# Performance work log

Hardware: AMD Instinct MI355X
Metric: run time of the kernel (lower is better)

Reference implementation:

```python
import jax, jax.numpy as jnp
import numpy as np

B, S, D, H, DQ, DK = 2, 2048, 1024, 16, 64, 64


def setup_inputs() -> dict:
    key = jax.random.key(0)
    ks = jax.random.split(key, 11)
    s = 0.02
    return {
        "query": jax.random.normal(ks[0], (B, S, D), jnp.float32),
        "key": jax.random.normal(ks[1], (B, S, D), jnp.float32),
        "value": jax.random.normal(ks[2], (B, S, D), jnp.float32),
        "Wq": jax.random.normal(ks[3], (H, D, DQ), jnp.float32) * s,
        "bq": jax.random.normal(ks[4], (H, DQ), jnp.float32) * s,
        "Wk": jax.random.normal(ks[5], (H, D, DK), jnp.float32) * s,
        "bk": jax.random.normal(ks[6], (H, DK), jnp.float32) * s,
        "Wv": jax.random.normal(ks[7], (H, D, DK), jnp.float32) * s,
        "bv": jax.random.normal(ks[8], (H, DK), jnp.float32) * s,
        "Wo": jax.random.normal(ks[9], (H * DK, D), jnp.float32) * s,
        "bo": jax.random.normal(ks[10], (D,), jnp.float32) * s,
    }


def reference(query, key, value, Wq, bq, Wk, bk, Wv, bv, Wo, bo):
    # Per-head linear projections (batched over heads): [B,H,S,dq/dk]
    q = jnp.einsum('bsd,hde->bhse', query, Wq) + bq[None, :, None, :]
    k = jnp.einsum('bsd,hde->bhse', key, Wk) + bk[None, :, None, :]
    v = jnp.einsum('bsd,hde->bhse', value, Wv) + bv[None, :, None, :]
    # Scaled dot-product attention: softmax(QK^T / sqrt(dim_q)) V
    scale = 1.0 / jnp.sqrt(jnp.asarray(q.shape[-1], q.dtype))
    scores = jnp.einsum('bhse,bhte->bhst', q, k) * scale  # [B,H,S,S]
    attn = jax.nn.softmax(scores, axis=-1)
    out = jnp.einsum('bhst,bhte->bhse', attn, v)  # [B,H,S,dk]
    # Concat heads along feature dim, then output linear
    cat = out.transpose(0, 2, 1, 3).reshape(out.shape[0], out.shape[2], -1)  # [B,S,H*dk]
    return cat @ Wo + bo
```

## Files before the change

### kernel.cpp

```cpp
#include <hip/hip_runtime.h>
#include <hip/hip_bf16.h>
#include <math.h>

#define NB 2
#define NS 2048
#define ND 1024
#define NH 16
#define DH 64
#define MROWS (NB*NS)
#define NCOLS (NH*DH)

typedef __attribute__((ext_vector_type(8))) short bf16x8;
typedef __attribute__((ext_vector_type(4))) float f32x4;
typedef __attribute__((ext_vector_type(16))) float f32x16;
typedef __attribute__((ext_vector_type(4))) unsigned short ushort4t;
typedef __attribute__((ext_vector_type(8))) unsigned short ushort8t;
typedef unsigned short ushort;

extern "C" __device__ float __ocml_native_exp2_f32(float);
#define EXP2F(x) __ocml_native_exp2_f32(x)
#define LOG2E 1.44269504088896f

static __device__ __forceinline__ ushort f2bf(float f) {
    union { __hip_bfloat16 b; ushort u; } cv;
    cv.b = __hip_bfloat16(f);
    return cv.u;
}

static __device__ __forceinline__ unsigned cvtpk(float a, float b) {
    unsigned r;
    asm("v_cvt_pk_bf16_f32 %0, %1, %2" : "=v"(r) : "v"(a), "v"(b));
    return r;
}

static __device__ __forceinline__ void gld_lds16(const void* g, void* l) {
    __builtin_amdgcn_global_load_lds(
        (const __attribute__((address_space(1))) void*)g,
        (__attribute__((address_space(3))) void*)l, 16, 0, 0);
}

__global__ __launch_bounds__(256) void convert_x(
    const float* __restrict__ q, const float* __restrict__ k,
    const float* __restrict__ v, ushort* __restrict__ X_bf)
{
    const size_t n1 = (size_t)MROWS * ND;
    const size_t off = ((size_t)blockIdx.x * 256 + threadIdx.x) * 8;
    const float* srcs[3] = {q, k, v};
    #pragma unroll
    for (int p = 0; p < 3; ++p) {
        float4 a = *(const float4*)(srcs[p] + off);
        float4 b = *(const float4*)(srcs[p] + off + 4);
        ushort8t w;
        w[0]=f2bf(a.x); w[1]=f2bf(a.y); w[2]=f2bf(a.z); w[3]=f2bf(a.w);
        w[4]=f2bf(b.x); w[5]=f2bf(b.y); w[6]=f2bf(b.z); w[7]=f2bf(b.w);
        *(ushort8t*)(X_bf + (size_t)p * n1 + off) = w;
    }
}

__global__ __launch_bounds__(256) void repack_w(
    const float* __restrict__ Wq, const float* __restrict__ Wk,
    const float* __restrict__ Wv, ushort* __restrict__ WT_bf)
{
    const int p = blockIdx.z;
    const float* W = (p == 0) ? Wq : (p == 1) ? Wk : Wv;
    const int h = blockIdx.y, d0 = blockIdx.x * 64;
    __shared__ float tile[64][65];
    const int t = threadIdx.x;
    {
        const int i = t >> 2, e0 = (t & 3) * 16;
        const float* src = W + ((size_t)h * ND + d0 + i) * DH + e0;
        #pragma unroll
        for (int u = 0; u < 4; ++u) {
            float4 v4 = ((const float4*)src)[u];
            tile[i][e0 + u*4 + 0] = v4.x; tile[i][e0 + u*4 + 1] = v4.y;
            tile[i][e0 + u*4 + 2] = v4.z; tile[i][e0 + u*4 + 3] = v4.w;
        }
    }
    __syncthreads();
    {
        const int e = t >> 2, dc = (t & 3) * 16;
        ushort* dst = WT_bf + ((size_t)p * NCOLS + h * 64 + e) * ND + d0 + dc;
        ushort8t w0, w1;
        #pragma unroll
        for (int u = 0; u < 8; ++u) { w0[u] = f2bf(tile[dc+u][e]); w1[u] = f2bf(tile[dc+8+u][e]); }
        *(ushort8t*)dst = w0;
        *(ushort8t*)(dst + 8) = w1;
    }
}

__global__ __launch_bounds__(256) void repack_wo(
    const float* __restrict__ Wo, ushort* __restrict__ WoT_bf)
{
    const int f0 = blockIdx.x * 64, c0 = blockIdx.y * 64;
    __shared__ float tile[64][65];
    const int t = threadIdx.x;
    {
        const int i = t >> 2, j0 = (t & 3) * 16;
        const float* src = Wo + (size_t)(f0 + i) * ND + c0 + j0;
        #pragma unroll
        for (int u = 0; u < 4; ++u) {
            float4 v4 = ((const float4*)src)[u];
            tile[i][j0 + u*4 + 0] = v4.x; tile[i][j0 + u*4 + 1] = v4.y;
            tile[i][j0 + u*4 + 2] = v4.z; tile[i][j0 + u*4 + 3] = v4.w;
        }
    }
    __syncthreads();
    {
        const int cl = t >> 2, fc = (t & 3) * 16;
        ushort* dst = WoT_bf + (size_t)(c0 + cl) * ND + f0 + fc;
        ushort8t w0, w1;
        #pragma unroll
        for (int u = 0; u < 8; ++u) { w0[u] = f2bf(tile[fc+u][cl]); w1[u] = f2bf(tile[fc+8+u][cl]); }
        *(ushort8t*)dst = w0;
        *(ushort8t*)(dst + 8) = w1;
    }
}

__global__ __launch_bounds__(256) void gemm_qkv(
    const ushort* __restrict__ X_bf, const ushort* __restrict__ WT_bf,
    const float* __restrict__ bq, const float* __restrict__ bk,
    const float* __restrict__ bv, ushort* __restrict__ qkv_bf)
{
    const int p = blockIdx.z;
    const float* bias = (p == 0) ? bq : (p == 1) ? bk : bv;
    const float scale = (p == 0) ? 0.125f * LOG2E : 1.0f;
    const int m0 = blockIdx.x * 128, n0 = blockIdx.y * 128;
    const int t = threadIdx.x, wid = t >> 6, lane = t & 63;
    const int wr = wid >> 1, wc = wid & 1;
    const int c = lane & 15, g = lane >> 4;

    __shared__ ushort ldsA[128 * 64];
    __shared__ ushort ldsB[128 * 64];

    const ushort* Ag = X_bf + (size_t)p * MROWS * ND + (size_t)m0 * ND;
    const ushort* Bg = WT_bf + (size_t)p * NCOLS * ND + (size_t)n0 * ND;

    f32x4 acc[4][4];
    #pragma unroll
    for (int m = 0; m < 4; ++m)
        #pragma unroll
        for (int n = 0; n < 4; ++n)
            acc[m][n] = (f32x4){0.f, 0.f, 0.f, 0.f};

    for (int k0 = 0; k0 < ND; k0 += 64) {
        __syncthreads();
        #pragma unroll
        for (int call = 0; call < 4; ++call) {
            const int chb = wid * 256 + call * 64;
            const int ch = chb + lane;
            const int row = ch >> 3, c16 = ch & 7;
            gld_lds16(Ag + (size_t)row * ND + k0 + c16 * 8, ldsA + (size_t)ch * 8);
            gld_lds16(Bg + (size_t)row * ND + k0 + c16 * 8, ldsB + (size_t)ch * 8);
        }
        __syncthreads();
        #pragma unroll
        for (int kc = 0; kc < 2; ++kc) {
            bf16x8 af[4], bfr[4];
            #pragma unroll
            for (int m = 0; m < 4; ++m)
                af[m] = *(const bf16x8*)(ldsA + (wr*64 + m*16 + c) * 64 + kc*32 + g*8);
            #pragma unroll
            for (int n = 0; n < 4; ++n)
                bfr[n] = *(const bf16x8*)(ldsB + (wc*64 + n*16 + c) * 64 + kc*32 + g*8);
            #pragma unroll
            for (int m = 0; m < 4; ++m)
                #pragma unroll
                for (int n = 0; n < 4; ++n)
                    acc[m][n] = __builtin_amdgcn_mfma_f32_16x16x32_bf16(af[m], bfr[n], acc[m][n], 0, 0, 0);
        }
    }

    ushort* dst = qkv_bf + (size_t)p * ((size_t)NB * NH * NS * DH);
    #pragma unroll
    for (int m = 0; m < 4; ++m) {
        const int gr0 = m0 + wr*64 + m*16 + g*4;
        #pragma unroll
        for (int n = 0; n < 4; ++n) {
            const int gc = n0 + wc*64 + n*16 + c;
            const int h = gc >> 6, e = gc & 63;
            const float bv_ = bias[gc];
            #pragma unroll
            for (int j = 0; j < 4; ++j) {
                const int r = gr0 + j;
                const int b = r >> 11, s = r & (NS - 1);
                dst[(((size_t)b * NH + h) * NS + s) * DH + e] = f2bf((acc[m][n][j] + bv_) * scale);
            }
        }
    }
}

__global__ __launch_bounds__(256) void v_transpose(
    const ushort* __restrict__ v_bf, ushort* __restrict__ vT_bf)
{
    const int bh = blockIdx.y, s0 = blockIdx.x * 256;
    __shared__ ushort tile[256][72];
    const int t = threadIdx.x;
    const ushort* src = v_bf + ((size_t)bh * NS + s0) * DH;
    #pragma unroll
    for (int u = 0; u < 8; ++u) {
        const int idx = u * 256 + t;
        const int row = idx >> 3, cc = (idx & 7) * 8;
        *(ushort8t*)&tile[row][cc] = *(const ushort8t*)(src + (size_t)row * DH + cc);
    }
    __syncthreads();
    const int e = t >> 2, sc = (t & 3) * 64;
    ushort* dst = vT_bf + ((size_t)bh * DH + e) * NS + s0 + sc;
    #pragma unroll
    for (int u = 0; u < 8; ++u) {
        ushort8t w;
        #pragma unroll
        for (int x = 0; x < 8; ++x) w[x] = tile[sc + u*8 + x][e];
        *(ushort8t*)(dst + u * 8) = w;
    }
}

__global__ __launch_bounds__(256) void attn_kernel(
    const ushort* __restrict__ q_bf, const ushort* __restrict__ k_bf,
    const ushort* __restrict__ vT_bf, ushort* __restrict__ cat_bf)
{
    __shared__ __attribute__((aligned(16))) char smem[32768];
    const int t = threadIdx.x;
    const int wid = t >> 6, lane = t & 63;
    const int ql = lane & 31;
    const int hi = lane >> 5;

    const int linear = blockIdx.x;
    const int xcd = linear & 7;
    const int idx = linear >> 3;
    const int bh = xcd * 4 + (idx >> 4);
    const int qx = idx & 15;
    const int qrow0 = qx * 128 + wid * 32;

    bf16x8 qf[4];
    {
        const char* qp = (const char*)(q_bf + ((size_t)bh * NS + qrow0 + ql) * DH);
        #pragma unroll
        for (int ds = 0; ds < 4; ++ds)
            qf[ds] = *(const bf16x8*)(qp + ds * 32 + hi * 16);
    }

    f32x16 o_acc[2];
    #pragma unroll
    for (int et = 0; et < 2; ++et)
        #pragma unroll
        for (int i = 0; i < 16; ++i)
            o_acc[et][i] = 0.f;
    float m = -INFINITY, lsum = 0.f;

    const char* kg = (const char*)(k_bf + (size_t)bh * NS * DH);
    const char* vg = (const char*)(vT_bf + (size_t)bh * DH * NS);

    const int ch0 = t * 2;
    const int row0 = ch0 >> 3, c16a = ch0 & 7;
    const int c16b = c16a + 1;
    const int swz0 = (c16a * 16) ^ ((row0 & 7) << 4);
    const int swz1 = (c16b * 16) ^ ((row0 & 7) << 4);

    ushort8t kr0, kr1, vr0, vr1;

    #define ATTN_LOAD(JT) do { \
        kr0 = *(const ushort8t*)(kg + (size_t)((JT) + row0) * 128 + c16a * 16); \
        kr1 = *(const ushort8t*)(kg + (size_t)((JT) + row0) * 128 + c16b * 16); \
        vr0 = *(const ushort8t*)(vg + (size_t)row0 * (NS*2) + (size_t)((JT) + c16a*8) * 2); \
        vr1 = *(const ushort8t*)(vg + (size_t)row0 * (NS*2) + (size_t)((JT) + c16b*8) * 2); \
    } while (0)

    #define ATTN_STORE(BUF) do { \
        char* Kd = smem + (BUF) * 8192; \
        char* Vd = smem + 16384 + (BUF) * 8192; \
        *(ushort8t*)(Kd + row0 * 128 + swz0) = kr0; \
        *(ushort8t*)(Kd + row0 * 128 + swz1) = kr1; \
        *(ushort8t*)(Vd + row0 * 128 + swz0) = vr0; \
        *(ushort8t*)(Vd + row0 * 128 + swz1) = vr1; \
    } while (0)

    ATTN_LOAD(0);
    ATTN_STORE(0);
    __syncthreads();
    int cur = 0;

    for (int jt = 0; jt < NS; jt += 64) {
        ATTN_LOAD((jt + 64) & (NS - 1));

        const char* Ks  = smem + cur * 8192;
        const char* VTs = smem + 16384 + cur * 8192;

        f32x16 s_acc[2];
        #pragma unroll
        for (int kt = 0; kt < 2; ++kt)
            #pragma unroll
            for (int i = 0; i < 16; ++i)
                s_acc[kt][i] = 0.f;
        __builtin_amdgcn_s_setprio(1);
        #pragma unroll
        for (int ds = 0; ds < 4; ++ds) {
            #pragma unroll
            for (int kt = 0; kt < 2; ++kt) {
                const int key = kt * 32 + ql;
                bf16x8 kf = *(const bf16x8*)(Ks + key * 128 + ((ds*32 + hi*16) ^ ((key & 7) << 4)));
                s_acc[kt] = __builtin_amdgcn_mfma_f32_32x32x16_bf16(kf, qf[ds], s_acc[kt], 0, 0, 0);
            }
        }
        __builtin_amdgcn_s_setprio(0);

        float tm = -INFINITY;
        #pragma unroll
        for (int kt = 0; kt < 2; ++kt)
            #pragma unroll
            for (int i = 0; i < 16; ++i)
                tm = fmaxf(tm, s_acc[kt][i]);
        if (!__all(tm <= m + 11.5f)) {
            const float tm2 = fmaxf(tm, __shfl_xor(tm, 32));
            const float mnew = fmaxf(m, tm2);
            const float sc = EXP2F(m - mnew);
            lsum *= sc;
            #pragma unroll
            for (int et = 0; et < 2; ++et)
                #pragma unroll
                for (int i = 0; i < 16; ++i)
                    o_acc[et][i] *= sc;
            m = mnew;
        }

        float rs = 0.f;
        #pragma unroll
        for (int kt = 0; kt < 2; ++kt) {
            float pe[16];
            #pragma unroll
            for (int i = 0; i < 16; ++i) {
                pe[i] = EXP2F(s_acc[kt][i] - m);
                rs += pe[i];
            }
            unsigned a0 = cvtpk(pe[0],  pe[1]);
            unsigned a1 = cvtpk(pe[2],  pe[3]);
            unsigned b0 = cvtpk(pe[4],  pe[5]);
            unsigned b1 = cvtpk(pe[6],  pe[7]);
            asm volatile("v_permlane32_swap_b32 %0, %1" : "+v"(a0), "+v"(b0));
            asm volatile("v_permlane32_swap_b32 %0, %1" : "+v"(a1), "+v"(b1));
            unsigned c0 = cvtpk(pe[8],  pe[9]);
            unsigned c1 = cvtpk(pe[10], pe[11]);
            unsigned d0 = cvtpk(pe[12], pe[13]);
            unsigned d1 = cvtpk(pe[14], pe[15]);
            asm volatile("v_permlane32_swap_b32 %0, %1" : "+v"(c0), "+v"(d0));
            asm volatile("v_permlane32_swap_b32 %0, %1" : "+v"(c1), "+v"(d1));
            union { bf16x8 v; unsigned u[4]; } B0, B1;
            B0.u[0] = a0; B0.u[1] = a1; B0.u[2] = b0; B0.u[3] = b1;
            B1.u[0] = c0; B1.u[1] = c1; B1.u[2] = d0; B1.u[3] = d1;

            __builtin_amdgcn_s_setprio(1);
            #pragma unroll
            for (int et = 0; et < 2; ++et) {
                const int e = et * 32 + ql;
                bf16x8 vf0 = *(const bf16x8*)(VTs + e * 128 + (((2*kt)   * 32 + hi*16) ^ ((e & 7) << 4)));
                o_acc[et] = __builtin_amdgcn_mfma_f32_32x32x16_bf16(vf0, B0.v, o_acc[et], 0, 0, 0);
                bf16x8 vf1 = *(const bf16x8*)(VTs + e * 128 + (((2*kt+1) * 32 + hi*16) ^ ((e & 7) << 4)));
                o_acc[et] = __builtin_amdgcn_mfma_f32_32x32x16_bf16(vf1, B1.v, o_acc[et], 0, 0, 0);
            }
            __builtin_amdgcn_s_setprio(0);
        }
        lsum += rs;

        ATTN_STORE(cur ^ 1);
        __syncthreads();
        cur ^= 1;
    }

    lsum += __shfl_xor(lsum, 32);
    const float inv = 1.0f / lsum;

    const int b = bh >> 4, hh = bh & 15;
    const int s = qrow0 + ql;
    ushort* op = cat_bf + ((size_t)b * NS + s) * NCOLS + hh * DH;
    #pragma unroll
    for (int et = 0; et < 2; ++et) {
        #pragma unroll
        for (int rgrp = 0; rgrp < 4; ++rgrp) {
            uint2 wv;
            wv.x = cvtpk(o_acc[et][rgrp*4+0] * inv, o_acc[et][rgrp*4+1] * inv);
            wv.y = cvtpk(o_acc[et][rgrp*4+2] * inv, o_acc[et][rgrp*4+3] * inv);
            *(uint2*)(op + et*32 + rgrp*8 + hi*4) = wv;
        }
    }
    #undef ATTN_LOAD
    #undef ATTN_STORE
}

__global__ __launch_bounds__(256) void gemm_out(
    const ushort* __restrict__ cat_bf, const ushort* __restrict__ WoT_bf,
    const float* __restrict__ bo, float* __restrict__ out)
{
    const int m0 = blockIdx.x * 128, n0 = blockIdx.y * 128;
    const int t = threadIdx.x, wid = t >> 6, lane = t & 63;
    const int wr = wid >> 1, wc = wid & 1;
    const int c = lane & 15, g = lane >> 4;

    __shared__ ushort ldsA[128 * 64];
    __shared__ ushort ldsB[128 * 64];

    const ushort* Ag = cat_bf + (size_t)m0 * ND;
    const ushort* Bg = WoT_bf + (size_t)n0 * ND;

    f32x4 acc[4][4];
    #pragma unroll
    for (int m = 0; m < 4; ++m)
        #pragma unroll
        for (int n = 0; n < 4; ++n)
            acc[m][n] = (f32x4){0.f, 0.f, 0.f, 0.f};

    for (int k0 = 0; k0 < ND; k0 += 64) {
        __syncthreads();
        #pragma unroll
        for (int call = 0; call < 4; ++call) {
            const int chb = wid * 256 + call * 64;
            const int ch = chb + lane;
            const int row = ch >> 3, c16 = ch & 7;
            gld_lds16(Ag + (size_t)row * ND + k0 + c16 * 8, ldsA + (size_t)ch * 8);
            gld_lds16(Bg + (size_t)row * ND + k0 + c16 * 8, ldsB + (size_t)ch * 8);
        }
        __syncthreads();
        #pragma unroll
        for (int kc = 0; kc < 2; ++kc) {
            bf16x8 af[4], bfr[4];
            #pragma unroll
            for (int m = 0; m < 4; ++m)
                af[m] = *(const bf16x8*)(ldsA + (wr*64 + m*16 + c) * 64 + kc*32 + g*8);
            #pragma unroll
            for (int n = 0; n < 4; ++n)
                bfr[n] = *(const bf16x8*)(ldsB + (wc*64 + n*16 + c) * 64 + kc*32 + g*8);
            #pragma unroll
            for (int m = 0; m < 4; ++m)
                #pragma unroll
                for (int n = 0; n < 4; ++n)
                    acc[m][n] = __builtin_amdgcn_mfma_f32_16x16x32_bf16(af[m], bfr[n], acc[m][n], 0, 0, 0);
        }
    }

    #pragma unroll
    for (int m = 0; m < 4; ++m) {
        const int gr0 = m0 + wr*64 + m*16 + g*4;
        #pragma unroll
        for (int n = 0; n < 4; ++n) {
            const int gc = n0 + wc*64 + n*16 + c;
            const float bv_ = bo[gc];
            #pragma unroll
            for (int j = 0; j < 4; ++j)
                out[(size_t)(gr0 + j) * ND + gc] = acc[m][n][j] + bv_;
        }
    }
}

extern "C" void kernel_launch(void* const* d_in, const int* in_sizes, int n_in,
                              void* d_out, int out_size, void* d_ws, size_t ws_size,
                              hipStream_t stream) {
    const float* query = (const float*)d_in[0];
    const float* key_  = (const float*)d_in[1];
    const float* value = (const float*)d_in[2];
    const float* Wq = (const float*)d_in[3];
    const float* bq = (const float*)d_in[4];
    const float* Wk = (const float*)d_in[5];
    const float* bk = (const float*)d_in[6];
    const float* Wv = (const float*)d_in[7];
    const float* bv = (const float*)d_in[8];
    const float* Wo = (const float*)d_in[9];
    const float* bo = (const float*)d_in[10];
    float* out = (float*)d_out;

    const size_t per = (size_t)NB * NH * NS * DH;
    const size_t xsz = (size_t)MROWS * ND;

    ushort* X_bf   = (ushort*)d_ws;
    ushort* qkv_bf = X_bf + 3 * xsz;
    ushort* vT_bf  = qkv_bf + 3 * per;
    ushort* WT_bf  = vT_bf + per;
    ushort* WoT_bf = WT_bf + (size_t)3 * ND * NCOLS;
    ushort* cat_bf = X_bf;

    convert_x<<<2048, 256, 0, stream>>>(query, key_, value, X_bf);
    repack_w<<<dim3(16, 16, 3), 256, 0, stream>>>(Wq, Wk, Wv, WT_bf);
    repack_wo<<<dim3(16, 16), 256, 0, stream>>>(Wo, WoT_bf);

    gemm_qkv<<<dim3(32, 8, 3), 256, 0, stream>>>(X_bf, WT_bf, bq, bk, bv, qkv_bf);
    v_transpose<<<dim3(8, 32), 256, 0, stream>>>(qkv_bf + 2 * per, vT_bf);

    attn_kernel<<<512, 256, 0, stream>>>(qkv_bf, qkv_bf + per, vT_bf, cat_bf);

    gemm_out<<<dim3(32, 8), 256, 0, stream>>>(cat_bf, WoT_bf, bo, out);
}
```

Before: 249.3 us.

## Fuse prep kernels, write V transposed from QKV GEMM, stage epilogue through LDS

The three conversion and repack kernels become one launch that dispatches on block index. The QKV GEMM now writes V directly in transposed layout with packed bf16 stores, which removes the separate v_transpose kernel and its extra pass over V. The Q/K epilogue is staged through LDS so global stores are 16-byte vectors instead of scattered 2-byte writes. The attention row-max reduction is rewritten with three-operand max. These cut launch overhead and memory traffic, at the cost of an extra LDS round trip and barriers in the GEMM epilogue.

```diff
diff --git a/kernel.cpp b/kernel.cpp
--- a/kernel.cpp
+++ b/kernel.cpp
@@ -13,7 +13,6 @@
 typedef __attribute__((ext_vector_type(8))) short bf16x8;
 typedef __attribute__((ext_vector_type(4))) float f32x4;
 typedef __attribute__((ext_vector_type(16))) float f32x16;
-typedef __attribute__((ext_vector_type(4))) unsigned short ushort4t;
 typedef __attribute__((ext_vector_type(8))) unsigned short ushort8t;
 typedef unsigned short ushort;
 
@@ -33,93 +32,97 @@
     return r;
 }
 
+static __device__ __forceinline__ float fmax3(float a, float b, float c) {
+    return fmaxf(fmaxf(a, b), c);
+}
+
 static __device__ __forceinline__ void gld_lds16(const void* g, void* l) {
     __builtin_amdgcn_global_load_lds(
         (const __attribute__((address_space(1))) void*)g,
         (__attribute__((address_space(3))) void*)l, 16, 0, 0);
 }
 
-__global__ __launch_bounds__(256) void convert_x(
+__global__ __launch_bounds__(256) void prep_kernel(
     const float* __restrict__ q, const float* __restrict__ k,
-    const float* __restrict__ v, ushort* __restrict__ X_bf)
-{
-    const size_t n1 = (size_t)MROWS * ND;
-    const size_t off = ((size_t)blockIdx.x * 256 + threadIdx.x) * 8;
-    const float* srcs[3] = {q, k, v};
-    #pragma unroll
-    for (int p = 0; p < 3; ++p) {
-        float4 a = *(const float4*)(srcs[p] + off);
-        float4 b = *(const float4*)(srcs[p] + off + 4);
-        ushort8t w;
-        w[0]=f2bf(a.x); w[1]=f2bf(a.y); w[2]=f2bf(a.z); w[3]=f2bf(a.w);
-        w[4]=f2bf(b.x); w[5]=f2bf(b.y); w[6]=f2bf(b.z); w[7]=f2bf(b.w);
-        *(ushort8t*)(X_bf + (size_t)p * n1 + off) = w;
-    }
-}
-
-__global__ __launch_bounds__(256) void repack_w(
+    const float* __restrict__ v, ushort* __restrict__ X_bf,
     const float* __restrict__ Wq, const float* __restrict__ Wk,
-    const float* __restrict__ Wv, ushort* __restrict__ WT_bf)
-{
-    const int p = blockIdx.z;
-    const float* W = (p == 0) ? Wq : (p == 1) ? Wk : Wv;
-    const int h = blockIdx.y, d0 = blockIdx.x * 64;
-    __shared__ float tile[64][65];
-    const int t = threadIdx.x;
-    {
-        const int i = t >> 2, e0 = (t & 3) * 16;
-        const float* src = W + ((size_t)h * ND + d0 + i) * DH + e0;
-        #pragma unroll
-        for (int u = 0; u < 4; ++u) {
-            float4 v4 = ((const float4*)src)[u];
-            tile[i][e0 + u*4 + 0] = v4.x; tile[i][e0 + u*4 + 1] = v4.y;
-            tile[i][e0 + u*4 + 2] = v4.z; tile[i][e0 + u*4 + 3] = v4.w;
-        }
-    }
-    __syncthreads();
-    {
-        const int e = t >> 2, dc = (t & 3) * 16;
-        ushort* dst = WT_bf + ((size_t)p * NCOLS + h * 64 + e) * ND + d0 + dc;
-        ushort8t w0, w1;
-        #pragma unroll
-        for (int u = 0; u < 8; ++u) { w0[u] = f2bf(tile[dc+u][e]); w1[u] = f2bf(tile[dc+8+u][e]); }
-        *(ushort8t*)dst = w0;
-        *(ushort8t*)(dst + 8) = w1;
-    }
-}
-
-__global__ __launch_bounds__(256) void repack_wo(
+    const float* __restrict__ Wv, ushort* __restrict__ WT_bf,
     const float* __restrict__ Wo, ushort* __restrict__ WoT_bf)
 {
-    const int f0 = blockIdx.x * 64, c0 = blockIdx.y * 64;
+    const int bx = blockIdx.x;
+    const int t = threadIdx.x;
     __shared__ float tile[64][65];
-    const int t = threadIdx.x;
-    {
-        const int i = t >> 2, j0 = (t & 3) * 16;
-        const float* src = Wo + (size_t)(f0 + i) * ND + c0 + j0;
-        #pragma unroll
-        for (int u = 0; u < 4; ++u) {
-            float4 v4 = ((const float4*)src)[u];
-            tile[i][j0 + u*4 + 0] = v4.x; tile[i][j0 + u*4 + 1] = v4.y;
-            tile[i][j0 + u*4 + 2] = v4.z; tile[i][j0 + u*4 + 3] = v4.w;
-        }
-    }
-    __syncthreads();
-    {
-        const int cl = t >> 2, fc = (t & 3) * 16;
-        ushort* dst = WoT_bf + (size_t)(c0 + cl) * ND + f0 + fc;
-        ushort8t w0, w1;
-        #pragma unroll
-        for (int u = 0; u < 8; ++u) { w0[u] = f2bf(tile[fc+u][cl]); w1[u] = f2bf(tile[fc+8+u][cl]); }
-        *(ushort8t*)dst = w0;
-        *(ushort8t*)(dst + 8) = w1;
+
+    if (bx < 2048) {
+        const size_t n1 = (size_t)MROWS * ND;
+        const size_t off = ((size_t)bx * 256 + t) * 8;
+        const float* srcs[3] = {q, k, v};
+        #pragma unroll
+        for (int p = 0; p < 3; ++p) {
+            float4 a = *(const float4*)(srcs[p] + off);
+            float4 b = *(const float4*)(srcs[p] + off + 4);
+            ushort8t w;
+            w[0]=f2bf(a.x); w[1]=f2bf(a.y); w[2]=f2bf(a.z); w[3]=f2bf(a.w);
+            w[4]=f2bf(b.x); w[5]=f2bf(b.y); w[6]=f2bf(b.z); w[7]=f2bf(b.w);
+            *(ushort8t*)(X_bf + (size_t)p * n1 + off) = w;
+        }
+    } else if (bx < 2816) {
+        const int i2 = bx - 2048;
+        const int p = i2 >> 8;
+        const int r = i2 & 255;
+        const int h = r >> 4, d0 = (r & 15) * 64;
+        const float* W = (p == 0) ? Wq : (p == 1) ? Wk : Wv;
+        {
+            const int i = t >> 2, e0 = (t & 3) * 16;
+            const float* src = W + ((size_t)h * ND + d0 + i) * DH + e0;
+            #pragma unroll
+            for (int u = 0; u < 4; ++u) {
+                float4 v4 = ((const float4*)src)[u];
+                tile[i][e0 + u*4 + 0] = v4.x; tile[i][e0 + u*4 + 1] = v4.y;
+                tile[i][e0 + u*4 + 2] = v4.z; tile[i][e0 + u*4 + 3] = v4.w;
+            }
+        }
+        __syncthreads();
+        {
+            const int e = t >> 2, dc = (t & 3) * 16;
+            ushort* dst = WT_bf + ((size_t)p * NCOLS + h * 64 + e) * ND + d0 + dc;
+            ushort8t w0, w1;
+            #pragma unroll
+            for (int u = 0; u < 8; ++u) { w0[u] = f2bf(tile[dc+u][e]); w1[u] = f2bf(tile[dc+8+u][e]); }
+            *(ushort8t*)dst = w0;
+            *(ushort8t*)(dst + 8) = w1;
+        }
+    } else {
+        const int i3 = bx - 2816;
+        const int f0 = (i3 & 15) * 64, c0 = (i3 >> 4) * 64;
+        {
+            const int i = t >> 2, j0 = (t & 3) * 16;
+            const float* src = Wo + (size_t)(f0 + i) * ND + c0 + j0;
+            #pragma unroll
+            for (int u = 0; u < 4; ++u) {
+                float4 v4 = ((const float4*)src)[u];
+                tile[i][j0 + u*4 + 0] = v4.x; tile[i][j0 + u*4 + 1] = v4.y;
+                tile[i][j0 + u*4 + 2] = v4.z; tile[i][j0 + u*4 + 3] = v4.w;
+            }
+        }
+        __syncthreads();
+        {
+            const int cl = t >> 2, fc = (t & 3) * 16;
+            ushort* dst = WoT_bf + (size_t)(c0 + cl) * ND + f0 + fc;
+            ushort8t w0, w1;
+            #pragma unroll
+            for (int u = 0; u < 8; ++u) { w0[u] = f2bf(tile[fc+u][cl]); w1[u] = f2bf(tile[fc+8+u][cl]); }
+            *(ushort8t*)dst = w0;
+            *(ushort8t*)(dst + 8) = w1;
+        }
     }
 }
 
 __global__ __launch_bounds__(256) void gemm_qkv(
     const ushort* __restrict__ X_bf, const ushort* __restrict__ WT_bf,
     const float* __restrict__ bq, const float* __restrict__ bk,
-    const float* __restrict__ bv, ushort* __restrict__ qkv_bf)
+    const float* __restrict__ bv, ushort* __restrict__ qkv_bf,
+    ushort* __restrict__ vT_bf)
 {
     const int p = blockIdx.z;
     const float* bias = (p == 0) ? bq : (p == 1) ? bk : bv;
@@ -129,8 +132,9 @@
     const int wr = wid >> 1, wc = wid & 1;
     const int c = lane & 15, g = lane >> 4;
 
-    __shared__ ushort ldsA[128 * 64];
-    __shared__ ushort ldsB[128 * 64];
+    __shared__ ushort ldsAB[2 * 128 * 64];
+    ushort* ldsA = ldsAB;
+    ushort* ldsB = ldsAB + 128 * 64;
 
     const ushort* Ag = X_bf + (size_t)p * MROWS * ND + (size_t)m0 * ND;
     const ushort* Bg = WT_bf + (size_t)p * NCOLS * ND + (size_t)n0 * ND;
@@ -146,8 +150,7 @@
         __syncthreads();
         #pragma unroll
         for (int call = 0; call < 4; ++call) {
-            const int chb = wid * 256 + call * 64;
-            const int ch = chb + lane;
+            const int ch = wid * 256 + call * 64 + lane;
             const int row = ch >> 3, c16 = ch & 7;
             gld_lds16(Ag + (size_t)row * ND + k0 + c16 * 8, ldsA + (size_t)ch * 8);
             gld_lds16(Bg + (size_t)row * ND + k0 + c16 * 8, ldsB + (size_t)ch * 8);
@@ -170,47 +173,51 @@
         }
     }
 
-    ushort* dst = qkv_bf + (size_t)p * ((size_t)NB * NH * NS * DH);
-    #pragma unroll
-    for (int m = 0; m < 4; ++m) {
-        const int gr0 = m0 + wr*64 + m*16 + g*4;
-        #pragma unroll
-        for (int n = 0; n < 4; ++n) {
-            const int gc = n0 + wc*64 + n*16 + c;
-            const int h = gc >> 6, e = gc & 63;
-            const float bv_ = bias[gc];
-            #pragma unroll
-            for (int j = 0; j < 4; ++j) {
-                const int r = gr0 + j;
-                const int b = r >> 11, s = r & (NS - 1);
-                dst[(((size_t)b * NH + h) * NS + s) * DH + e] = f2bf((acc[m][n][j] + bv_) * scale);
-            }
-        }
-    }
-}
-
-__global__ __launch_bounds__(256) void v_transpose(
-    const ushort* __restrict__ v_bf, ushort* __restrict__ vT_bf)
-{
-    const int bh = blockIdx.y, s0 = blockIdx.x * 256;
-    __shared__ ushort tile[256][72];
-    const int t = threadIdx.x;
-    const ushort* src = v_bf + ((size_t)bh * NS + s0) * DH;
-    #pragma unroll
-    for (int u = 0; u < 8; ++u) {
-        const int idx = u * 256 + t;
-        const int row = idx >> 3, cc = (idx & 7) * 8;
-        *(ushort8t*)&tile[row][cc] = *(const ushort8t*)(src + (size_t)row * DH + cc);
-    }
-    __syncthreads();
-    const int e = t >> 2, sc = (t & 3) * 64;
-    ushort* dst = vT_bf + ((size_t)bh * DH + e) * NS + s0 + sc;
-    #pragma unroll
-    for (int u = 0; u < 8; ++u) {
-        ushort8t w;
-        #pragma unroll
-        for (int x = 0; x < 8; ++x) w[x] = tile[sc + u*8 + x][e];
-        *(ushort8t*)(dst + u * 8) = w;
+    if (p == 2) {
+        #pragma unroll
+        for (int m = 0; m < 4; ++m) {
+            const int s0b = m0 + wr*64 + m*16 + g*4;
+            const int b = s0b >> 11, sl = s0b & (NS - 1);
+            #pragma unroll
+            for (int n = 0; n < 4; ++n) {
+                const int gc = n0 + wc*64 + n*16 + c;
+                const int h = gc >> 6, e = gc & 63;
+                const float bv_ = bias[gc];
+                uint2 wv;
+                wv.x = cvtpk(acc[m][n][0] + bv_, acc[m][n][1] + bv_);
+                wv.y = cvtpk(acc[m][n][2] + bv_, acc[m][n][3] + bv_);
+                *(uint2*)(vT_bf + ((size_t)(b * NH + h) * DH + e) * NS + sl) = wv;
+            }
+        }
+    } else {
+        __syncthreads();
+        ushort* ldsC = ldsAB;
+        #pragma unroll
+        for (int m = 0; m < 4; ++m)
+            #pragma unroll
+            for (int n = 0; n < 4; ++n) {
+                const int col = wc*64 + n*16 + c;
+                const float bv_ = bias[n0 + col];
+                #pragma unroll
+                for (int j = 0; j < 4; ++j) {
+                    const int row = wr*64 + m*16 + g*4 + j;
+                    ldsC[row * 128 + col] = f2bf((acc[m][n][j] + bv_) * scale);
+                }
+            }
+        __syncthreads();
+        ushort* dstbase = qkv_bf + (size_t)p * ((size_t)NB * NH * NS * DH);
+        #pragma unroll
+        for (int rr = 0; rr < 8; ++rr) {
+            const int idx = rr * 256 + t;
+            const int row = idx >> 4;
+            const int col0 = (idx & 15) * 8;
+            const int gc = n0 + col0;
+            const int h = gc >> 6, e0 = gc & 63;
+            const int gr = m0 + row;
+            const int b = gr >> 11, s = gr & (NS - 1);
+            ushort8t w = *(ushort8t*)(ldsC + row * 128 + col0);
+            *(ushort8t*)(dstbase + (((size_t)b * NH + h) * NS + s) * DH + e0) = w;
+        }
     }
 }
 
@@ -303,12 +310,11 @@
         }
         __builtin_amdgcn_s_setprio(0);
 
-        float tm = -INFINITY;
-        #pragma unroll
-        for (int kt = 0; kt < 2; ++kt)
-            #pragma unroll
-            for (int i = 0; i < 16; ++i)
-                tm = fmaxf(tm, s_acc[kt][i]);
+        float tm = fmaxf(s_acc[0][0], s_acc[0][1]);
+        #pragma unroll
+        for (int i = 2; i < 16; i += 2) tm = fmax3(tm, s_acc[0][i], s_acc[0][i+1]);
+        #pragma unroll
+        for (int i = 0; i < 16; i += 2) tm = fmax3(tm, s_acc[1][i], s_acc[1][i+1]);
         if (!__all(tm <= m + 11.5f)) {
             const float tm2 = fmaxf(tm, __shfl_xor(tm, 32));
             const float mnew = fmaxf(m, tm2);
@@ -411,8 +417,7 @@
         __syncthreads();
         #pragma unroll
         for (int call = 0; call < 4; ++call) {
-            const int chb = wid * 256 + call * 64;
-            const int ch = chb + lane;
+            const int ch = wid * 256 + call * 64 + lane;
             const int row = ch >> 3, c16 = ch & 7;
             gld_lds16(Ag + (size_t)row * ND + k0 + c16 * 8, ldsA + (size_t)ch * 8);
             gld_lds16(Bg + (size_t)row * ND + k0 + c16 * 8, ldsB + (size_t)ch * 8);
@@ -475,12 +480,10 @@
     ushort* WoT_bf = WT_bf + (size_t)3 * ND * NCOLS;
     ushort* cat_bf = X_bf;
 
-    convert_x<<<2048, 256, 0, stream>>>(query, key_, value, X_bf);
-    repack_w<<<dim3(16, 16, 3), 256, 0, stream>>>(Wq, Wk, Wv, WT_bf);
-    repack_wo<<<dim3(16, 16), 256, 0, stream>>>(Wo, WoT_bf);
-
-    gemm_qkv<<<dim3(32, 8, 3), 256, 0, stream>>>(X_bf, WT_bf, bq, bk, bv, qkv_bf);
-    v_transpose<<<dim3(8, 32), 256, 0, stream>>>(qkv_bf + 2 * per, vT_bf);
+    prep_kernel<<<3072, 256, 0, stream>>>(query, key_, value, X_bf,
+                                          Wq, Wk, Wv, WT_bf, Wo, WoT_bf);
+
+    gemm_qkv<<<dim3(32, 8, 3), 256, 0, stream>>>(X_bf, WT_bf, bq, bk, bv, qkv_bf, vT_bf);
 
     attn_kernel<<<512, 256, 0, stream>>>(qkv_bf, qkv_bf + per, vT_bf, cat_bf);
 
```

Result: faster. 238.5 us (-4.3%).
